# Kernel optimization log

Hardware: AMD Instinct MI355X
Metric: run time of the kernel (lower is better)

Reference implementation:

```python
import jax, jax.numpy as jnp
import numpy as np

H = 16  # attention heads


def _layer_norm(x, g, b, eps=1e-5):
    m = jnp.mean(x, axis=-1, keepdims=True)
    v = jnp.var(x, axis=-1, keepdims=True)
    return (x - m) * jax.lax.rsqrt(v + eps) * g + b


def _attn(q_in, k_in, wq, bq, wk, bk, wv, bv, wo, bo, h=H):
    # q_in, k_in: (L, N, E); weights: (inner_dim, E); causal mask always applied
    L, N, E = q_in.shape
    D = wq.shape[0]
    d = D // h
    scale = jnp.float32(d) ** -0.5
    q = (q_in @ wq.T + bq).reshape(L, N * h, d).transpose(1, 0, 2) * scale  # (N*h, L, d)
    k = (k_in @ wk.T + bk).reshape(L, N * h, d).transpose(1, 0, 2)
    v = (k_in @ wv.T + bv).reshape(L, N * h, d).transpose(1, 0, 2)
    s = jnp.einsum('bld,bmd->blm', q, k)  # (N*h, L, L)
    causal = jnp.tril(jnp.ones((L, L), dtype=bool))
    s = jnp.where(causal, s, jnp.float32(-10000.0))  # masked_fill with -10000.0
    a = jax.nn.softmax(s, axis=-1)
    o = jnp.einsum('blm,bmd->bld', a, v)  # (N*h, L, d)
    o = o.transpose(1, 0, 2).reshape(L, N, D)
    return o @ wo.T + bo


def setup_inputs() -> dict:
    key = jax.random.key(0)
    L, N, E, F = 1024, 4, 1024, 4096
    ks = iter(jax.random.split(key, 40))

    def nrm(shape, s=0.02):
        return (jax.random.normal(next(ks), shape, jnp.float32) * s).astype(jnp.float32)

    inp = {
        'x': nrm((L, N, E), 1.0),
        'encoder_out': nrm((L, N, E), 1.0),
        # self-attention
        'wq_s': nrm((E, E)), 'bq_s': jnp.zeros((E,), jnp.float32),
        'wk_s': nrm((E, E)), 'bk_s': jnp.zeros((E,), jnp.float32),
        'wv_s': nrm((E, E)), 'bv_s': jnp.zeros((E,), jnp.float32),
        'wo_s': nrm((E, E)), 'bo_s': jnp.zeros((E,), jnp.float32),
        # encoder-decoder attention
        'wq_c': nrm((E, E)), 'bq_c': jnp.zeros((E,), jnp.float32),
        'wk_c': nrm((E, E)), 'bk_c': jnp.zeros((E,), jnp.float32),
        'wv_c': nrm((E, E)), 'bv_c': jnp.zeros((E,), jnp.float32),
        'wo_c': nrm((E, E)), 'bo_c': jnp.zeros((E,), jnp.float32),
        # layer norms
        'ln1_g': jnp.ones((E,), jnp.float32), 'ln1_b': jnp.zeros((E,), jnp.float32),
        'ln2_g': jnp.ones((E,), jnp.float32), 'ln2_b': jnp.zeros((E,), jnp.float32),
        'ln3_g': jnp.ones((E,), jnp.float32), 'ln3_b': jnp.zeros((E,), jnp.float32),
        # FFN
        'fc1_w': nrm((F, E)), 'fc1_b': jnp.zeros((F,), jnp.float32),
        'fc2_w': nrm((E, F)), 'fc2_b': jnp.zeros((E,), jnp.float32),
    }
    return inp


def reference(x, encoder_out,
              wq_s, bq_s, wk_s, bk_s, wv_s, bv_s, wo_s, bo_s,
              wq_c, bq_c, wk_c, bk_c, wv_c, bv_c, wo_c, bo_c,
              ln1_g, ln1_b, ln2_g, ln2_b, ln3_g, ln3_b,
              fc1_w, fc1_b, fc2_w, fc2_b):
    # DecoderLayer.forward (pre-LN, dropout p=0 for determinism)
    residual = x
    h = _layer_norm(x, ln1_g, ln1_b)
    x = residual + _attn(h, h, wq_s, bq_s, wk_s, bk_s, wv_s, bv_s, wo_s, bo_s)

    residual = x
    h = _layer_norm(x, ln2_g, ln2_b)
    x = residual + _attn(h, encoder_out, wq_c, bq_c, wk_c, bk_c, wv_c, bv_c, wo_c, bo_c)

    residual = x
    h = _layer_norm(x, ln3_g, ln3_b)
    h = jax.nn.gelu(h @ fc1_w.T + fc1_b, approximate=False)  # torch F.gelu (erf)
    x = residual + (h @ fc2_w.T + fc2_b)
    return x
```

## Files before the change

### kernel.cpp

```cpp
#include <hip/hip_runtime.h>
#include <stdint.h>

#define LSEQ   1024
#define NBATCH 4
#define EDIM   1024
#define FDIM   4096
#define MROWS  (LSEQ * NBATCH)
#define NHEAD  16
#define DHEAD  64

typedef unsigned short bf16_t;
typedef __attribute__((ext_vector_type(8))) short  short8;
typedef __attribute__((ext_vector_type(4))) float  floatx4;

__device__ __forceinline__ bf16_t f2bf(float f) {
    unsigned u = __float_as_uint(f);
    u += 0x7FFFu + ((u >> 16) & 1u);
    return (bf16_t)(u >> 16);
}

__global__ void cvt_f32_bf16(const float* __restrict__ in, bf16_t* __restrict__ out, int n4) {
    int i = blockIdx.x * blockDim.x + threadIdx.x;
    if (i >= n4) return;
    float4 v = ((const float4*)in)[i];
    uint2 pk;
    pk.x = (unsigned)f2bf(v.x) | ((unsigned)f2bf(v.y) << 16);
    pk.y = (unsigned)f2bf(v.z) | ((unsigned)f2bf(v.w) << 16);
    ((uint2*)out)[i] = pk;
}

__global__ void cvt2_f32_bf16(const float* __restrict__ a, const float* __restrict__ b,
                              bf16_t* __restrict__ da, bf16_t* __restrict__ db) {
    const int n4 = (FDIM * EDIM) / 4;
    int i = blockIdx.x * blockDim.x + threadIdx.x;
    if (i >= n4) return;
    const float* src = (blockIdx.y == 0) ? a : b;
    bf16_t* out = (blockIdx.y == 0) ? da : db;
    float4 v = ((const float4*)src)[i];
    uint2 pk;
    pk.x = (unsigned)f2bf(v.x) | ((unsigned)f2bf(v.y) << 16);
    pk.y = (unsigned)f2bf(v.z) | ((unsigned)f2bf(v.w) << 16);
    ((uint2*)out)[i] = pk;
}

__global__ void cvt3_f32_bf16(const float* __restrict__ a, const float* __restrict__ b,
                              const float* __restrict__ c, bf16_t* __restrict__ dst) {
    const int n4 = (EDIM * EDIM) / 4;
    int i = blockIdx.x * blockDim.x + threadIdx.x;
    if (i >= n4) return;
    const float* src = (blockIdx.y == 0) ? a : (blockIdx.y == 1) ? b : c;
    bf16_t* out = dst + (size_t)blockIdx.y * EDIM * EDIM;
    float4 v = ((const float4*)src)[i];
    uint2 pk;
    pk.x = (unsigned)f2bf(v.x) | ((unsigned)f2bf(v.y) << 16);
    pk.y = (unsigned)f2bf(v.z) | ((unsigned)f2bf(v.w) << 16);
    ((uint2*)out)[i] = pk;
}

__global__ void ln_row(const float* __restrict__ x, const float* __restrict__ g,
                       const float* __restrict__ b, bf16_t* __restrict__ out) {
    int row = blockIdx.x, tid = threadIdx.x;
    const float* xr = x + (size_t)row * EDIM;
    float4 v = *(const float4*)(xr + tid * 4);
    float s = v.x + v.y + v.z + v.w;
    float q = v.x * v.x + v.y * v.y + v.z * v.z + v.w * v.w;
#pragma unroll
    for (int off = 32; off > 0; off >>= 1) {
        s += __shfl_xor(s, off);
        q += __shfl_xor(q, off);
    }
    __shared__ float ss[4], sq[4];
    int w = tid >> 6;
    if ((tid & 63) == 0) { ss[w] = s; sq[w] = q; }
    __syncthreads();
    s = ss[0] + ss[1] + ss[2] + ss[3];
    q = sq[0] + sq[1] + sq[2] + sq[3];
    float mean = s * (1.0f / EDIM);
    float var  = q * (1.0f / EDIM) - mean * mean;
    float rstd = rsqrtf(var + 1e-5f);
    int c = tid * 4;
    float4 gv = *(const float4*)(g + c);
    float4 bv = *(const float4*)(b + c);
    uint2 pk;
    pk.x = (unsigned)f2bf((v.x - mean) * rstd * gv.x + bv.x)
         | ((unsigned)f2bf((v.y - mean) * rstd * gv.y + bv.y) << 16);
    pk.y = (unsigned)f2bf((v.z - mean) * rstd * gv.z + bv.z)
         | ((unsigned)f2bf((v.w - mean) * rstd * gv.w + bv.w) << 16);
    *(uint2*)(out + (size_t)row * EDIM + c) = pk;
}


template<int ROWS, int NW>
__device__ __forceinline__ void stage_async(const bf16_t* __restrict__ G, int rBase,
                                            int k0, int ld, bf16_t* s, int wv, int lane) {
#pragma unroll
    for (int i = 0; i < ROWS / (8 * NW); i++) {
        int c = wv + i * NW;
        int row = c * 8 + (lane >> 3);
        int slog = (lane & 7) ^ (row & 7);
        const bf16_t* g = G + (size_t)(rBase + row) * ld + k0 + slog * 8;
        bf16_t* l = s + c * 512;
        __builtin_amdgcn_global_load_lds(
            (const __attribute__((address_space(1))) void*)g,
            (__attribute__((address_space(3))) void*)l, 16, 0, 0);
    }
}

template<int ROWS, int NT>
__device__ __forceinline__ void stage_f32_sw(const float* __restrict__ A, int rBase,
                                             int k0, int ld, bf16_t* s, int tid) {
#pragma unroll
    for (int i = 0; i < ROWS * 16 / NT; i++) {
        int ch = tid + i * NT;
        int row = ch >> 4, q4 = ch & 15;
        float4 v = *(const float4*)(A + (size_t)(rBase + row) * ld + k0 + q4 * 4);
        uint2 pk;
        pk.x = (unsigned)f2bf(v.x) | ((unsigned)f2bf(v.y) << 16);
        pk.y = (unsigned)f2bf(v.z) | ((unsigned)f2bf(v.w) << 16);
        int slog = q4 >> 1, half = q4 & 1;
        *(uint2*)(s + row * 64 + ((slog ^ (row & 7)) * 8) + half * 4) = pk;
    }
}

__device__ __forceinline__ short8 frag_ld(const bf16_t* s, int row, int kk, int quad) {
    return *(const short8*)(s + row * 64 + (((kk << 2) | quad) ^ (row & 7)) * 8);
}

template<int BMt>
__global__ __launch_bounds__(512, 4) void gemm_bt(
    const void* __restrict__ Ap, int aIsF32,
    const void* __restrict__ Wp, int wIsBf16,
    const float* __restrict__ bias, const float* __restrict__ res,
    void* __restrict__ outp, int K,
    int lda, int ldw, int ldo, int mode, float scale)
{
    constexpr int MT = BMt / 32;
    __shared__ __align__(16) bf16_t sA[BMt * 64];
    __shared__ __align__(16) bf16_t sW[128 * 64];
    int tid  = threadIdx.x;
    int wv   = tid >> 6, lane = tid & 63;
    int col  = lane & 15, quad = lane >> 4;
    int wm   = wv >> 2,  wn   = wv & 3;
    int mBase = blockIdx.y * BMt;
    int nBase = blockIdx.x * 128;

    floatx4 acc[MT][2];
#pragma unroll
    for (int i = 0; i < MT; i++)
#pragma unroll
        for (int j = 0; j < 2; j++) acc[i][j] = (floatx4){0.f, 0.f, 0.f, 0.f};

    for (int k0 = 0; k0 < K; k0 += 64) {
        if (aIsF32) stage_f32_sw<BMt, 512>((const float*)Ap, mBase, k0, lda, sA, tid);
        else        stage_async<BMt, 8>((const bf16_t*)Ap, mBase, k0, lda, sA, wv, lane);
        if (wIsBf16) stage_async<128, 8>((const bf16_t*)Wp, nBase, k0, ldw, sW, wv, lane);
        else         stage_f32_sw<128, 512>((const float*)Wp, nBase, k0, ldw, sW, tid);
        __syncthreads();
#pragma unroll
        for (int kk = 0; kk < 2; kk++) {
            short8 aF[MT], bF[2];
#pragma unroll
            for (int mt = 0; mt < MT; mt++)
                aF[mt] = frag_ld(sA, wm * (BMt / 2) + mt * 16 + col, kk, quad);
#pragma unroll
            for (int nt = 0; nt < 2; nt++)
                bF[nt] = frag_ld(sW, wn * 32 + nt * 16 + col, kk, quad);
#pragma unroll
            for (int mt = 0; mt < MT; mt++)
#pragma unroll
                for (int nt = 0; nt < 2; nt++)
                    acc[mt][nt] = __builtin_amdgcn_mfma_f32_16x16x32_bf16(aF[mt], bF[nt], acc[mt][nt], 0, 0, 0);
        }
        __syncthreads();
    }

#pragma unroll
    for (int mt = 0; mt < MT; mt++) {
#pragma unroll
        for (int nt = 0; nt < 2; nt++) {
            int gc = nBase + wn * 32 + nt * 16 + col;
            float bsv = bias ? bias[gc] : 0.0f;
#pragma unroll
            for (int r = 0; r < 4; r++) {
                int gr = mBase + wm * (BMt / 2) + mt * 16 + quad * 4 + r;
                float val = acc[mt][nt][r] + bsv;
                size_t idx = (size_t)gr * ldo + gc;
                if (mode == 0) {
                    ((bf16_t*)outp)[idx] = f2bf(val * scale);
                } else if (mode == 1) {
                    ((float*)outp)[idx] = res[idx] + val;
                } else {
                    float gl = 0.5f * val * (1.0f + erff(val * 0.70710678118654752f));
                    ((bf16_t*)outp)[idx] = f2bf(gl);
                }
            }
        }
    }
}

template<int DUMMY>
__global__ __launch_bounds__(256, 3) void gemm_bt4(
    const void* __restrict__ Ap, int aIsF32,
    const void* __restrict__ Wp, int wIsBf16,
    const float* __restrict__ bias, const float* __restrict__ res,
    void* __restrict__ outp, int K,
    int lda, int ldw, int ldo, int mode, float scale)
{
    __shared__ __align__(16) bf16_t sA[128 * 64];
    __shared__ __align__(16) bf16_t sW[128 * 64];
    int tid  = threadIdx.x;
    int wv   = tid >> 6, lane = tid & 63;
    int col  = lane & 15, quad = lane >> 4;
    int wm   = wv >> 1,  wn   = wv & 1;
    int mBase = blockIdx.y * 128;
    int nBase = blockIdx.x * 128;

    floatx4 acc[4][4];
#pragma unroll
    for (int i = 0; i < 4; i++)
#pragma unroll
        for (int j = 0; j < 4; j++) acc[i][j] = (floatx4){0.f, 0.f, 0.f, 0.f};

    for (int k0 = 0; k0 < K; k0 += 64) {
        if (aIsF32) stage_f32_sw<128, 256>((const float*)Ap, mBase, k0, lda, sA, tid);
        else        stage_async<128, 4>((const bf16_t*)Ap, mBase, k0, lda, sA, wv, lane);
        if (wIsBf16) stage_async<128, 4>((const bf16_t*)Wp, nBase, k0, ldw, sW, wv, lane);
        else         stage_f32_sw<128, 256>((const float*)Wp, nBase, k0, ldw, sW, tid);
        __syncthreads();
#pragma unroll
        for (int kk = 0; kk < 2; kk++) {
            short8 aF[4], bF[4];
#pragma unroll
            for (int mt = 0; mt < 4; mt++)
                aF[mt] = frag_ld(sA, wm * 64 + mt * 16 + col, kk, quad);
#pragma unroll
            for (int nt = 0; nt < 4; nt++)
                bF[nt] = frag_ld(sW, wn * 64 + nt * 16 + col, kk, quad);
#pragma unroll
            for (int mt = 0; mt < 4; mt++)
#pragma unroll
                for (int nt = 0; nt < 4; nt++)
                    acc[mt][nt] = __builtin_amdgcn_mfma_f32_16x16x32_bf16(aF[mt], bF[nt], acc[mt][nt], 0, 0, 0);
        }
        __syncthreads();
    }

#pragma unroll
    for (int mt = 0; mt < 4; mt++) {
#pragma unroll
        for (int nt = 0; nt < 4; nt++) {
            int gc = nBase + wn * 64 + nt * 16 + col;
            float bsv = bias ? bias[gc] : 0.0f;
#pragma unroll
            for (int r = 0; r < 4; r++) {
                int gr = mBase + wm * 64 + mt * 16 + quad * 4 + r;
                float val = acc[mt][nt][r] + bsv;
                size_t idx = (size_t)gr * ldo + gc;
                if (mode == 0) {
                    ((bf16_t*)outp)[idx] = f2bf(val * scale);
                } else if (mode == 1) {
                    ((float*)outp)[idx] = res[idx] + val;
                } else {
                    float gl = 0.5f * val * (1.0f + erff(val * 0.70710678118654752f));
                    ((bf16_t*)outp)[idx] = f2bf(gl);
                }
            }
        }
    }
}

__global__ __launch_bounds__(256, 3) void gemm_qkv4(
    const void* __restrict__ A0, int f0, const void* __restrict__ A12, int f12,
    const void* __restrict__ Wq, const void* __restrict__ Wk, const void* __restrict__ Wv,
    int wIsBf16,
    const float* __restrict__ bq, const float* __restrict__ bk, const float* __restrict__ bv,
    bf16_t* __restrict__ oq, bf16_t* __restrict__ ok, bf16_t* __restrict__ ovT,
    float qscale)
{
    __shared__ __align__(16) bf16_t sA[128 * 64];
    __shared__ __align__(16) bf16_t sW[128 * 64];
    int tid  = threadIdx.x;
    int wv   = tid >> 6, lane = tid & 63;
    int col  = lane & 15, quad = lane >> 4;
    int wm   = wv >> 1,  wn   = wv & 1;
    int seg  = blockIdx.x >> 3;
    int nBase = (blockIdx.x & 7) * 128;
    int mBase = blockIdx.y * 128;

    const void* Ap     = (seg == 0) ? A0 : A12;
    int         aIsF32 = (seg == 0) ? f0 : f12;
    const void* W      = (seg == 0) ? Wq : (seg == 1) ? Wk : Wv;
    const float* bias  = (seg == 0) ? bq : (seg == 1) ? bk : bv;
    float       scale  = (seg == 0) ? qscale : 1.0f;

    floatx4 acc[4][4];
#pragma unroll
    for (int i = 0; i < 4; i++)
#pragma unroll
        for (int j = 0; j < 4; j++) acc[i][j] = (floatx4){0.f, 0.f, 0.f, 0.f};

    for (int k0 = 0; k0 < EDIM; k0 += 64) {
        if (aIsF32) stage_f32_sw<128, 256>((const float*)Ap, mBase, k0, EDIM, sA, tid);
        else        stage_async<128, 4>((const bf16_t*)Ap, mBase, k0, EDIM, sA, wv, lane);
        if (wIsBf16) stage_async<128, 4>((const bf16_t*)W, nBase, k0, EDIM, sW, wv, lane);
        else         stage_f32_sw<128, 256>((const float*)W, nBase, k0, EDIM, sW, tid);
        __syncthreads();
#pragma unroll
        for (int kk = 0; kk < 2; kk++) {
            short8 aF[4], bF[4];
#pragma unroll
            for (int mt = 0; mt < 4; mt++)
                aF[mt] = frag_ld(sA, wm * 64 + mt * 16 + col, kk, quad);
#pragma unroll
            for (int nt = 0; nt < 4; nt++)
                bF[nt] = frag_ld(sW, wn * 64 + nt * 16 + col, kk, quad);
#pragma unroll
            for (int mt = 0; mt < 4; mt++)
#pragma unroll
                for (int nt = 0; nt < 4; nt++)
                    acc[mt][nt] = __builtin_amdgcn_mfma_f32_16x16x32_bf16(aF[mt], bF[nt], acc[mt][nt], 0, 0, 0);
        }
        __syncthreads();
    }

#pragma unroll
    for (int mt = 0; mt < 4; mt++) {
#pragma unroll
        for (int nt = 0; nt < 4; nt++) {
            int gc = nBase + wn * 64 + nt * 16 + col;
            float bsv = bias[gc];
#pragma unroll
            for (int r = 0; r < 4; r++) {
                int gr = mBase + wm * 64 + mt * 16 + quad * 4 + r;
                float val = acc[mt][nt][r] + bsv;
                if (seg == 2) {
                    int nb = gr & 3, l = gr >> 2;
                    ovT[((size_t)(nb * EDIM) + gc) * LSEQ + l] = f2bf(val);
                } else {
                    bf16_t* out = (seg == 0) ? oq : ok;
                    out[(size_t)gr * EDIM + gc] = f2bf(val * scale);
                }
            }
        }
    }
}

__device__ __forceinline__ void attn_tile(
    short8 aQ0, short8 aQ1, short8 b00, short8 b01, short8 b10, short8 b11,
    const short8* bV, int qbase, int k0, int col, int quad,
    floatx4* accO, float* ls, bf16_t* myP)
{
    floatx4 zero = {0.f, 0.f, 0.f, 0.f};
    floatx4 S0 = zero, S1 = zero;
    S0 = __builtin_amdgcn_mfma_f32_16x16x32_bf16(aQ0, b00, S0, 0, 0, 0);
    S0 = __builtin_amdgcn_mfma_f32_16x16x32_bf16(aQ1, b01, S0, 0, 0, 0);
    S1 = __builtin_amdgcn_mfma_f32_16x16x32_bf16(aQ0, b10, S1, 0, 0, 0);
    S1 = __builtin_amdgcn_mfma_f32_16x16x32_bf16(aQ1, b11, S1, 0, 0, 0);

#pragma unroll
    for (int r = 0; r < 4; r++) {
        int qrow = qbase + quad * 4 + r;
        float e0 = ((k0 + col)      > qrow) ? 0.0f : __expf(S0[r]);
        float e1 = ((k0 + 16 + col) > qrow) ? 0.0f : __expf(S1[r]);
        ls[r] += e0 + e1;
        myP[(quad * 4 + r) * 32 + col]      = f2bf(e0);
        myP[(quad * 4 + r) * 32 + col + 16] = f2bf(e1);
    }
    asm volatile("" ::: "memory");
    short8 aP = *(const short8*)(myP + col * 32 + quad * 8);
#pragma unroll
    for (int nt = 0; nt < 4; nt++)
        accO[nt] = __builtin_amdgcn_mfma_f32_16x16x32_bf16(aP, bV[nt], accO[nt], 0, 0, 0);
}

__global__ __launch_bounds__(256, 2) void flash_attn(
    const bf16_t* Q, const bf16_t* __restrict__ Kt,
    const bf16_t* __restrict__ Vt, bf16_t* O)
{
    __shared__ bf16_t sP[4][2][16 * 32];
    int tid = threadIdx.x;
    int wv = tid >> 6, lane = tid & 63;
    int col = lane & 15, quad = lane >> 4;
    int bh = blockIdx.x;
    int n = bh >> 4, head = bh & 15;
    int t1 = blockIdx.y * 4 + wv;
    int t2 = 63 - t1;
    int q1 = t1 * 16, q2 = t2 * 16;

    const bf16_t* Kb = Kt + (size_t)n * EDIM + head * DHEAD + quad * 8;
    const bf16_t* Vb = Vt + ((size_t)n * EDIM + head * DHEAD) * LSEQ;

    size_t q1off = ((size_t)(q1 + col) * NBATCH + n) * EDIM + head * DHEAD + quad * 8;
    size_t q2off = ((size_t)(q2 + col) * NBATCH + n) * EDIM + head * DHEAD + quad * 8;
    short8 aQ10 = *(const short8*)(Q + q1off);
    short8 aQ11 = *(const short8*)(Q + q1off + 32);
    short8 aQ20 = *(const short8*)(Q + q2off);
    short8 aQ21 = *(const short8*)(Q + q2off + 32);

    floatx4 zero = {0.f, 0.f, 0.f, 0.f};
    floatx4 accO1[4], accO2[4];
#pragma unroll
    for (int i = 0; i < 4; i++) { accO1[i] = zero; accO2[i] = zero; }
    float ls1[4] = {0.f, 0.f, 0.f, 0.f};
    float ls2[4] = {0.f, 0.f, 0.f, 0.f};

    int nT1 = (q1 + 47) >> 5;
    int nT2 = (q2 + 47) >> 5;
    for (int t = 0; t < nT2; t++) {
        int k0 = t * 32;
        const bf16_t* kr0 = Kb + (size_t)(k0 + col) * EDIM * NBATCH;
        const bf16_t* kr1 = Kb + (size_t)(k0 + 16 + col) * EDIM * NBATCH;
        short8 b00 = *(const short8*)kr0;
        short8 b01 = *(const short8*)(kr0 + 32);
        short8 b10 = *(const short8*)kr1;
        short8 b11 = *(const short8*)(kr1 + 32);
        short8 bV[4];
#pragma unroll
        for (int nt = 0; nt < 4; nt++)
            bV[nt] = *(const short8*)(Vb + (size_t)(nt * 16 + col) * LSEQ + k0 + quad * 8);

        attn_tile(aQ20, aQ21, b00, b01, b10, b11, bV, q2, k0, col, quad,
                  accO2, ls2, sP[wv][1]);
        if (t < nT1)
            attn_tile(aQ10, aQ11, b00, b01, b10, b11, bV, q1, k0, col, quad,
                      accO1, ls1, sP[wv][0]);
    }
#pragma unroll
    for (int r = 0; r < 4; r++) {
#pragma unroll
        for (int off = 1; off < 16; off <<= 1) {
            ls1[r] += __shfl_xor(ls1[r], off);
            ls2[r] += __shfl_xor(ls2[r], off);
        }
    }
#pragma unroll
    for (int r = 0; r < 4; r++) {
        float inv1 = 1.0f / ls1[r];
        float inv2 = 1.0f / ls2[r];
        size_t base1 = ((size_t)(q1 + quad * 4 + r) * NBATCH + n) * EDIM + head * DHEAD;
        size_t base2 = ((size_t)(q2 + quad * 4 + r) * NBATCH + n) * EDIM + head * DHEAD;
#pragma unroll
        for (int nt = 0; nt < 4; nt++) {
            O[base1 + nt * 16 + col] = f2bf(accO1[nt][r] * inv1);
            O[base2 + nt * 16 + col] = f2bf(accO2[nt][r] * inv2);
        }
    }
}

extern "C" void kernel_launch(void* const* d_in, const int* in_sizes, int n_in,
                              void* d_out, int out_size, void* d_ws, size_t ws_size,
                              hipStream_t stream) {
    const float* x    = (const float*)d_in[0];
    const float* enc  = (const float*)d_in[1];
    const float* wq_s = (const float*)d_in[2];  const float* bq_s = (const float*)d_in[3];
    const float* wk_s = (const float*)d_in[4];  const float* bk_s = (const float*)d_in[5];
    const float* wv_s = (const float*)d_in[6];  const float* bv_s = (const float*)d_in[7];
    const float* wo_s = (const float*)d_in[8];  const float* bo_s = (const float*)d_in[9];
    const float* wq_c = (const float*)d_in[10]; const float* bq_c = (const float*)d_in[11];
    const float* wk_c = (const float*)d_in[12]; const float* bk_c = (const float*)d_in[13];
    const float* wv_c = (const float*)d_in[14]; const float* bv_c = (const float*)d_in[15];
    const float* wo_c = (const float*)d_in[16]; const float* bo_c = (const float*)d_in[17];
    const float* ln1_g = (const float*)d_in[18]; const float* ln1_b = (const float*)d_in[19];
    const float* ln2_g = (const float*)d_in[20]; const float* ln2_b = (const float*)d_in[21];
    const float* ln3_g = (const float*)d_in[22]; const float* ln3_b = (const float*)d_in[23];
    const float* fc1_w = (const float*)d_in[24]; const float* fc1_b = (const float*)d_in[25];
    const float* fc2_w = (const float*)d_in[26]; const float* fc2_b = (const float*)d_in[27];
    float* outF = (float*)d_out;

    char* wsb = (char*)d_ws;
    bf16_t* hA  = (bf16_t*)(wsb);
    bf16_t* qB  = (bf16_t*)(wsb + ((size_t)8  << 20));
    bf16_t* kC  = (bf16_t*)(wsb + ((size_t)16 << 20));
    bf16_t* vD  = (bf16_t*)(wsb + ((size_t)24 << 20));
    bf16_t* mid = qB;
    float*  xr  = outF;

    const bool fast = ws_size >= ((size_t)48 << 20);
    bf16_t* encbf = fast ? (bf16_t*)(wsb + ((size_t)32 << 20)) : nullptr;
    bf16_t* wbuf  = fast ? (bf16_t*)(wsb + ((size_t)40 << 20)) : nullptr;

    const float qscale = 0.125f;
    const int Fh = FDIM / 2;
    const int EE = EDIM * EDIM;
    dim3 attnGrid(NBATCH * NHEAD, 8);
    dim3 qkvGrid(24, MROWS / 128);
    dim3 cvtW((EE / 4 + 255) / 256, 3);

    ln_row<<<MROWS, 256, 0, stream>>>(x, ln1_g, ln1_b, hA);
    if (fast) {
        cvt3_f32_bf16<<<cvtW, 256, 0, stream>>>(wq_s, wk_s, wv_s, wbuf);
        cvt_f32_bf16<<<(MROWS * EDIM / 4 + 255) / 256, 256, 0, stream>>>(enc, encbf, MROWS * EDIM / 4);
        gemm_qkv4<<<qkvGrid, 256, 0, stream>>>(hA, 0, hA, 0,
                                               wbuf, wbuf + EE, wbuf + 2 * EE, 1,
                                               bq_s, bk_s, bv_s, qB, kC, vD, qscale);
    } else {
        gemm_qkv4<<<qkvGrid, 256, 0, stream>>>(hA, 0, hA, 0,
                                               wq_s, wk_s, wv_s, 0,
                                               bq_s, bk_s, bv_s, qB, kC, vD, qscale);
    }
    flash_attn<<<attnGrid, 256, 0, stream>>>(qB, kC, vD, qB);
    if (fast) {
        cvt_f32_bf16<<<(EE / 4 + 255) / 256, 256, 0, stream>>>(wo_s, wbuf, EE / 4);
        gemm_bt<64><<<dim3(8, 64), 512, 0, stream>>>(qB, 0, wbuf, 1, bo_s, x, xr,
                                                     EDIM, EDIM, EDIM, EDIM, 1, 1.0f);
    } else {
        gemm_bt<64><<<dim3(8, 64), 512, 0, stream>>>(qB, 0, wo_s, 0, bo_s, x, xr,
                                                     EDIM, EDIM, EDIM, EDIM, 1, 1.0f);
    }

    ln_row<<<MROWS, 256, 0, stream>>>(xr, ln2_g, ln2_b, hA);
    if (fast) {
        cvt3_f32_bf16<<<cvtW, 256, 0, stream>>>(wq_c, wk_c, wv_c, wbuf);
        gemm_qkv4<<<qkvGrid, 256, 0, stream>>>(hA, 0, encbf, 0,
                                               wbuf, wbuf + EE, wbuf + 2 * EE, 1,
                                               bq_c, bk_c, bv_c, qB, kC, vD, qscale);
    } else {
        gemm_qkv4<<<qkvGrid, 256, 0, stream>>>(hA, 0, enc, 1,
                                               wq_c, wk_c, wv_c, 0,
                                               bq_c, bk_c, bv_c, qB, kC, vD, qscale);
    }
    flash_attn<<<attnGrid, 256, 0, stream>>>(qB, kC, vD, qB);
    if (fast) {
        cvt_f32_bf16<<<(EE / 4 + 255) / 256, 256, 0, stream>>>(wo_c, wbuf, EE / 4);
        gemm_bt<64><<<dim3(8, 64), 512, 0, stream>>>(qB, 0, wbuf, 1, bo_c, xr, xr,
                                                     EDIM, EDIM, EDIM, EDIM, 1, 1.0f);
    } else {
        gemm_bt<64><<<dim3(8, 64), 512, 0, stream>>>(qB, 0, wo_c, 0, bo_c, xr, xr,
                                                     EDIM, EDIM, EDIM, EDIM, 1, 1.0f);
    }

    ln_row<<<MROWS, 256, 0, stream>>>(xr, ln3_g, ln3_b, hA);
    if (fast) {
        cvt2_f32_bf16<<<dim3((FDIM * EDIM / 4 + 255) / 256, 2), 256, 0, stream>>>(
            fc1_w, fc2_w, wbuf, encbf);
        for (int h = 0; h < 2; h++) {
            const float* b2 = (h == 1) ? fc2_b : nullptr;
            gemm_bt4<0><<<dim3(Fh / 128, 32), 256, 0, stream>>>(
                hA, 0, wbuf + (size_t)h * Fh * EDIM, 1, fc1_b + h * Fh, nullptr, mid,
                EDIM, EDIM, EDIM, Fh, 2, 1.0f);
            gemm_bt<64><<<dim3(8, 64), 512, 0, stream>>>(
                mid, 0, encbf + (size_t)h * Fh, 1, b2, xr, xr,
                Fh, Fh, FDIM, EDIM, 1, 1.0f);
        }
    } else {
        for (int h = 0; h < 2; h++) {
            const float* b2 = (h == 1) ? fc2_b : nullptr;
            gemm_bt4<0><<<dim3(Fh / 128, 32), 256, 0, stream>>>(
                hA, 0, fc1_w + (size_t)h * Fh * EDIM, 0, fc1_b + h * Fh, nullptr, mid,
                EDIM, EDIM, EDIM, Fh, 2, 1.0f);
            gemm_bt<64><<<dim3(8, 64), 512, 0, stream>>>(
                mid, 0, fc2_w + (size_t)h * Fh, 0, b2, xr, xr,
                Fh, Fh, FDIM, EDIM, 1, 1.0f);
        }
    }
}
```

Measured before the change: 576.8 us.

## Split attention KV range across wave pairs and merge partials in LDS

Flash attention now launches 512 threads per block. Each pair of waves splits the key tiles of its two query tiles in half, and the two partial output accumulators and row sums are merged through shared memory before the final normalization. This is meant to double parallelism and shorten the serial KV loop per wave. It costs extra LDS, a block-wide barrier and duplicated K/V loads. The P scratch buffer is also padded to stride 36 to reduce LDS bank conflicts, and the wo weight conversion is folded into the QKV conversion launch to remove a kernel launch.

Result: slower. 603.3 us (+4.6%).

```diff
diff --git a/kernel.cpp b/kernel.cpp
--- a/kernel.cpp
+++ b/kernel.cpp
@@ -8,6 +8,7 @@
 #define MROWS  (LSEQ * NBATCH)
 #define NHEAD  16
 #define DHEAD  64
+#define PPAD   36
 
 typedef unsigned short bf16_t;
 typedef __attribute__((ext_vector_type(8))) short  short8;
@@ -17,16 +18,6 @@
     unsigned u = __float_as_uint(f);
     u += 0x7FFFu + ((u >> 16) & 1u);
     return (bf16_t)(u >> 16);
-}
-
-__global__ void cvt_f32_bf16(const float* __restrict__ in, bf16_t* __restrict__ out, int n4) {
-    int i = blockIdx.x * blockDim.x + threadIdx.x;
-    if (i >= n4) return;
-    float4 v = ((const float4*)in)[i];
-    uint2 pk;
-    pk.x = (unsigned)f2bf(v.x) | ((unsigned)f2bf(v.y) << 16);
-    pk.y = (unsigned)f2bf(v.z) | ((unsigned)f2bf(v.w) << 16);
-    ((uint2*)out)[i] = pk;
 }
 
 __global__ void cvt2_f32_bf16(const float* __restrict__ a, const float* __restrict__ b,
@@ -43,14 +34,26 @@
     ((uint2*)out)[i] = pk;
 }
 
-__global__ void cvt3_f32_bf16(const float* __restrict__ a, const float* __restrict__ b,
-                              const float* __restrict__ c, bf16_t* __restrict__ dst) {
+__global__ void cvt4_f32_bf16(const float* __restrict__ a, const float* __restrict__ b,
+                              const float* __restrict__ c, const float* __restrict__ d,
+                              bf16_t* __restrict__ dst) {
     const int n4 = (EDIM * EDIM) / 4;
     int i = blockIdx.x * blockDim.x + threadIdx.x;
     if (i >= n4) return;
-    const float* src = (blockIdx.y == 0) ? a : (blockIdx.y == 1) ? b : c;
+    const float* src = (blockIdx.y == 0) ? a : (blockIdx.y == 1) ? b
+                     : (blockIdx.y == 2) ? c : d;
     bf16_t* out = dst + (size_t)blockIdx.y * EDIM * EDIM;
     float4 v = ((const float4*)src)[i];
+    uint2 pk;
+    pk.x = (unsigned)f2bf(v.x) | ((unsigned)f2bf(v.y) << 16);
+    pk.y = (unsigned)f2bf(v.z) | ((unsigned)f2bf(v.w) << 16);
+    ((uint2*)out)[i] = pk;
+}
+
+__global__ void cvt_f32_bf16(const float* __restrict__ in, bf16_t* __restrict__ out, int n4) {
+    int i = blockIdx.x * blockDim.x + threadIdx.x;
+    if (i >= n4) return;
+    float4 v = ((const float4*)in)[i];
     uint2 pk;
     pk.x = (unsigned)f2bf(v.x) | ((unsigned)f2bf(v.y) << 16);
     pk.y = (unsigned)f2bf(v.z) | ((unsigned)f2bf(v.w) << 16);
@@ -89,7 +92,6 @@
     *(uint2*)(out + (size_t)row * EDIM + c) = pk;
 }
 
-
 template<int ROWS, int NW>
 __device__ __forceinline__ void stage_async(const bf16_t* __restrict__ G, int rBase,
                                             int k0, int ld, bf16_t* s, int wv, int lane) {
@@ -363,27 +365,29 @@
         float e0 = ((k0 + col)      > qrow) ? 0.0f : __expf(S0[r]);
         float e1 = ((k0 + 16 + col) > qrow) ? 0.0f : __expf(S1[r]);
         ls[r] += e0 + e1;
-        myP[(quad * 4 + r) * 32 + col]      = f2bf(e0);
-        myP[(quad * 4 + r) * 32 + col + 16] = f2bf(e1);
+        myP[(quad * 4 + r) * PPAD + col]      = f2bf(e0);
+        myP[(quad * 4 + r) * PPAD + col + 16] = f2bf(e1);
     }
     asm volatile("" ::: "memory");
-    short8 aP = *(const short8*)(myP + col * 32 + quad * 8);
+    short8 aP = *(const short8*)(myP + col * PPAD + quad * 8);
 #pragma unroll
     for (int nt = 0; nt < 4; nt++)
         accO[nt] = __builtin_amdgcn_mfma_f32_16x16x32_bf16(aP, bV[nt], accO[nt], 0, 0, 0);
 }
 
-__global__ __launch_bounds__(256, 2) void flash_attn(
+__global__ __launch_bounds__(512, 2) void flash_attn(
     const bf16_t* Q, const bf16_t* __restrict__ Kt,
     const bf16_t* __restrict__ Vt, bf16_t* O)
 {
-    __shared__ bf16_t sP[4][2][16 * 32];
+    __shared__ bf16_t sP[8][2][16 * PPAD];
+    __shared__ __align__(16) float sM[4][64][40];
     int tid = threadIdx.x;
     int wv = tid >> 6, lane = tid & 63;
     int col = lane & 15, quad = lane >> 4;
+    int pairId = wv >> 1, half = wv & 1;
     int bh = blockIdx.x;
     int n = bh >> 4, head = bh & 15;
-    int t1 = blockIdx.y * 4 + wv;
+    int t1 = blockIdx.y * 4 + pairId;
     int t2 = 63 - t1;
     int q1 = t1 * 16, q2 = t2 * 16;
 
@@ -406,7 +410,10 @@
 
     int nT1 = (q1 + 47) >> 5;
     int nT2 = (q2 + 47) >> 5;
-    for (int t = 0; t < nT2; t++) {
+    int s1 = half ? (nT1 >> 1) : 0, e1 = half ? nT1 : (nT1 >> 1);
+    int s2 = half ? (nT2 >> 1) : 0, e2 = half ? nT2 : (nT2 >> 1);
+
+    for (int t = s2; t < e2; t++) {
         int k0 = t * 32;
         const bf16_t* kr0 = Kb + (size_t)(k0 + col) * EDIM * NBATCH;
         const bf16_t* kr1 = Kb + (size_t)(k0 + 16 + col) * EDIM * NBATCH;
@@ -418,12 +425,44 @@
 #pragma unroll
         for (int nt = 0; nt < 4; nt++)
             bV[nt] = *(const short8*)(Vb + (size_t)(nt * 16 + col) * LSEQ + k0 + quad * 8);
-
         attn_tile(aQ20, aQ21, b00, b01, b10, b11, bV, q2, k0, col, quad,
                   accO2, ls2, sP[wv][1]);
-        if (t < nT1)
-            attn_tile(aQ10, aQ11, b00, b01, b10, b11, bV, q1, k0, col, quad,
-                      accO1, ls1, sP[wv][0]);
+    }
+    for (int t = s1; t < e1; t++) {
+        int k0 = t * 32;
+        const bf16_t* kr0 = Kb + (size_t)(k0 + col) * EDIM * NBATCH;
+        const bf16_t* kr1 = Kb + (size_t)(k0 + 16 + col) * EDIM * NBATCH;
+        short8 b00 = *(const short8*)kr0;
+        short8 b01 = *(const short8*)(kr0 + 32);
+        short8 b10 = *(const short8*)kr1;
+        short8 b11 = *(const short8*)(kr1 + 32);
+        short8 bV[4];
+#pragma unroll
+        for (int nt = 0; nt < 4; nt++)
+            bV[nt] = *(const short8*)(Vb + (size_t)(nt * 16 + col) * LSEQ + k0 + quad * 8);
+        attn_tile(aQ10, aQ11, b00, b01, b10, b11, bV, q1, k0, col, quad,
+                  accO1, ls1, sP[wv][0]);
+    }
+
+    if (half) {
+        float* m = sM[pairId][lane];
+#pragma unroll
+        for (int i = 0; i < 4; i++) *(floatx4*)(m + i * 4)      = accO1[i];
+#pragma unroll
+        for (int i = 0; i < 4; i++) *(floatx4*)(m + 16 + i * 4) = accO2[i];
+#pragma unroll
+        for (int r = 0; r < 4; r++) { m[32 + r] = ls1[r]; m[36 + r] = ls2[r]; }
+    }
+    __syncthreads();
+    if (half) return;
+    {
+        const float* m = sM[pairId][lane];
+#pragma unroll
+        for (int i = 0; i < 4; i++) accO1[i] += *(const floatx4*)(m + i * 4);
+#pragma unroll
+        for (int i = 0; i < 4; i++) accO2[i] += *(const floatx4*)(m + 16 + i * 4);
+#pragma unroll
+        for (int r = 0; r < 4; r++) { ls1[r] += m[32 + r]; ls2[r] += m[36 + r]; }
     }
 #pragma unroll
     for (int r = 0; r < 4; r++) {
@@ -484,11 +523,11 @@
     const int EE = EDIM * EDIM;
     dim3 attnGrid(NBATCH * NHEAD, 8);
     dim3 qkvGrid(24, MROWS / 128);
-    dim3 cvtW((EE / 4 + 255) / 256, 3);
+    dim3 cvtW((EE / 4 + 255) / 256, 4);
 
     ln_row<<<MROWS, 256, 0, stream>>>(x, ln1_g, ln1_b, hA);
     if (fast) {
-        cvt3_f32_bf16<<<cvtW, 256, 0, stream>>>(wq_s, wk_s, wv_s, wbuf);
+        cvt4_f32_bf16<<<cvtW, 256, 0, stream>>>(wq_s, wk_s, wv_s, wo_s, wbuf);
         cvt_f32_bf16<<<(MROWS * EDIM / 4 + 255) / 256, 256, 0, stream>>>(enc, encbf, MROWS * EDIM / 4);
         gemm_qkv4<<<qkvGrid, 256, 0, stream>>>(hA, 0, hA, 0,
                                                wbuf, wbuf + EE, wbuf + 2 * EE, 1,
@@ -498,10 +537,9 @@
                                                wq_s, wk_s, wv_s, 0,
                                                bq_s, bk_s, bv_s, qB, kC, vD, qscale);
     }
-    flash_attn<<<attnGrid, 256, 0, stream>>>(qB, kC, vD, qB);
+    flash_attn<<<attnGrid, 512, 0, stream>>>(qB, kC, vD, qB);
     if (fast) {
-        cvt_f32_bf16<<<(EE / 4 + 255) / 256, 256, 0, stream>>>(wo_s, wbuf, EE / 4);
-        gemm_bt<64><<<dim3(8, 64), 512, 0, stream>>>(qB, 0, wbuf, 1, bo_s, x, xr,
+        gemm_bt<64><<<dim3(8, 64), 512, 0, stream>>>(qB, 0, wbuf + 3 * (size_t)EE, 1, bo_s, x, xr,
                                                      EDIM, EDIM, EDIM, EDIM, 1, 1.0f);
     } else {
         gemm_bt<64><<<dim3(8, 64), 512, 0, stream>>>(qB, 0, wo_s, 0, bo_s, x, xr,
@@ -510,7 +548,7 @@
 
     ln_row<<<MROWS, 256, 0, stream>>>(xr, ln2_g, ln2_b, hA);
     if (fast) {
-        cvt3_f32_bf16<<<cvtW, 256, 0, stream>>>(wq_c, wk_c, wv_c, wbuf);
+        cvt4_f32_bf16<<<cvtW, 256, 0, stream>>>(wq_c, wk_c, wv_c, wo_c, wbuf);
         gemm_qkv4<<<qkvGrid, 256, 0, stream>>>(hA, 0, encbf, 0,
                                                wbuf, wbuf + EE, wbuf + 2 * EE, 1,
                                                bq_c, bk_c, bv_c, qB, kC, vD, qscale);
@@ -519,10 +557,9 @@
                                                wq_c, wk_c, wv_c, 0,
                                                bq_c, bk_c, bv_c, qB, kC, vD, qscale);
     }
-    flash_attn<<<attnGrid, 256, 0, stream>>>(qB, kC, vD, qB);
+    flash_attn<<<attnGrid, 512, 0, stream>>>(qB, kC, vD, qB);
     if (fast) {
-        cvt_f32_bf16<<<(EE / 4 + 255) / 256, 256, 0, stream>>>(wo_c, wbuf, EE / 4);
-        gemm_bt<64><<<dim3(8, 64), 512, 0, stream>>>(qB, 0, wbuf, 1, bo_c, xr, xr,
+        gemm_bt<64><<<dim3(8, 64), 512, 0, stream>>>(qB, 0, wbuf + 3 * (size_t)EE, 1, bo_c, xr, xr,
                                                      EDIM, EDIM, EDIM, EDIM, 1, 1.0f);
     } else {
         gemm_bt<64><<<dim3(8, 64), 512, 0, stream>>>(qB, 0, wo_c, 0, bo_c, xr, xr,
```
